# Performance work log

Measured on AMD Instinct MI355X. Metric: run time of the kernel, lower is better.

Reference implementation:

```python
import jax, jax.numpy as jnp
import numpy as np

N_NODES = 100000
N_EDGES = 1600000
IN_DIM = 128
HIDDEN = 128


def setup_inputs() -> dict:
    key = jax.random.key(0)
    k1, k2, k3 = jax.random.split(key, 3)
    x = jax.random.normal(k1, (N_NODES, IN_DIM), dtype=jnp.float32)
    edge_index = jax.random.randint(k2, (2, N_EDGES), 0, N_NODES, dtype=jnp.int64)
    # Glorot-ish init for the GCN weight
    W = jax.random.normal(k3, (IN_DIM, HIDDEN), dtype=jnp.float32) * (1.0 / np.sqrt(IN_DIM))
    b = jnp.zeros((HIDDEN,), dtype=jnp.float32)
    return {"x": x, "edge_index": edge_index, "W": W, "b": b}


def reference(x, edge_index, W, b):
    N = x.shape[0]
    # PyG GCNConv: add self-loops, symmetric deg^{-1/2} normalization,
    # linear transform, scatter-add aggregation at destination, + bias.
    loop = jnp.arange(N, dtype=edge_index.dtype)
    src = jnp.concatenate([edge_index[0], loop])
    dst = jnp.concatenate([edge_index[1], loop])

    ones = jnp.ones(src.shape[0], dtype=x.dtype)
    deg = jax.ops.segment_sum(ones, dst, num_segments=N)  # in-degree incl. self-loop
    dinv = jnp.where(deg > 0, jax.lax.rsqrt(deg), 0.0)
    norm = dinv[src] * dinv[dst]  # [E+N]

    xw = x @ W  # [N, H] dense transform first (GCNConv default)
    msgs = xw[src] * norm[:, None]  # gather + scale, [E+N, H]
    out = jax.ops.segment_sum(msgs, dst, num_segments=N) + b  # scatter-add
    return jax.nn.relu(out)
```

## Files before the change

### kernel.cpp

```cpp
#include <hip/hip_runtime.h>
#include <hip/hip_bf16.h>


#define SCAN_BLK 256
#define NP1 128
#define MAXB 1024

typedef short  short8 __attribute__((ext_vector_type(8)));
typedef float  f32x4  __attribute__((ext_vector_type(4)));

__device__ inline unsigned short f2b(float f) {
    unsigned u = __float_as_uint(f);
    return (unsigned short)((u + 0x7fffu + ((u >> 16) & 1u)) >> 16);
}

__device__ inline void acc4(float4& a, unsigned lo, unsigned hi) {
    a.x += __uint_as_float(lo << 16);
    a.y += __uint_as_float(lo & 0xffff0000u);
    a.z += __uint_as_float(hi << 16);
    a.w += __uint_as_float(hi & 0xffff0000u);
}

__global__ __launch_bounds__(256) void k_hist(const int* __restrict__ dst,
                                              int* __restrict__ hist,
                                              const float* __restrict__ W,
                                              unsigned short* __restrict__ Wt,
                                              int E, int B, int chunk) {
    __shared__ int h[MAXB];
    for (int i = threadIdx.x; i < B; i += 256) h[i] = 0;
    __syncthreads();
    int e0 = blockIdx.x * chunk;
    int e1 = min(E, e0 + chunk);
    for (int e = e0 + threadIdx.x; e < e1; e += 256)
        atomicAdd(&h[dst[e] >> 7], 1);
    __syncthreads();
    for (int i = threadIdx.x; i < B; i += 256)
        hist[i * NP1 + blockIdx.x] = h[i];
    if (blockIdx.x < 64) {
        int i = blockIdx.x * 256 + threadIdx.x;
        int k = i >> 7, n = i & 127;
        Wt[n * 128 + k] = f2b(W[k * 128 + n]);
    }
}

__global__ __launch_bounds__(SCAN_BLK) void k_scanA(const int* __restrict__ in,
                                                    int* __restrict__ bsum, int M) {
    __shared__ int s[SCAN_BLK];
    int t = threadIdx.x;
    int i = blockIdx.x * SCAN_BLK + t;
    s[t] = (i < M) ? in[i] : 0;
    __syncthreads();
    for (int off = SCAN_BLK / 2; off > 0; off >>= 1) {
        if (t < off) s[t] += s[t + off];
        __syncthreads();
    }
    if (t == 0) bsum[blockIdx.x] = s[0];
}

__global__ __launch_bounds__(512) void k_scanB(int* __restrict__ bsum, int nb) {
    __shared__ int s[512];
    int t = threadIdx.x;
    int v = (t < nb) ? bsum[t] : 0;
    s[t] = v;
    __syncthreads();
    for (int off = 1; off < 512; off <<= 1) {
        int add = (t >= off) ? s[t - off] : 0;
        __syncthreads();
        s[t] += add;
        __syncthreads();
    }
    if (t < nb) bsum[t] = s[t] - v;
}

__global__ __launch_bounds__(SCAN_BLK) void k_scanC2(int* __restrict__ data,
                                                     const int* __restrict__ bsum,
                                                     int M) {
    __shared__ int s[SCAN_BLK];
    int t = threadIdx.x;
    int i = blockIdx.x * SCAN_BLK + t;
    int v = (i < M) ? data[i] : 0;
    s[t] = v;
    __syncthreads();
    for (int off = 1; off < SCAN_BLK; off <<= 1) {
        int add = (t >= off) ? s[t - off] : 0;
        __syncthreads();
        s[t] += add;
        __syncthreads();
    }
    if (i < M) data[i] = s[t] - v + bsum[blockIdx.x];
}

__global__ __launch_bounds__(256) void k_scatter(const int* __restrict__ src,
                                                 const int* __restrict__ dst,
                                                 const int* __restrict__ hist_s,
                                                 unsigned* __restrict__ bucketed,
                                                 int E, int B, int chunk) {
    __shared__ int cur[MAXB];
    for (int i = threadIdx.x; i < B; i += 256)
        cur[i] = hist_s[i * NP1 + blockIdx.x];
    __syncthreads();
    int e0 = blockIdx.x * chunk;
    int e1 = min(E, e0 + chunk);
    for (int e = e0 + threadIdx.x; e < e1; e += 256) {
        int d = dst[e];
        int p = atomicAdd(&cur[d >> 7], 1);
        bucketed[p] = (unsigned)src[e] | ((unsigned)(d & 127) << 17);
    }
}

__global__ __launch_bounds__(256) void k_csr(const unsigned* __restrict__ bucketed,
                                             const int* __restrict__ hist_s,
                                             int* __restrict__ csr_src,
                                             int* __restrict__ rowptr,
                                             float* __restrict__ dinv_g,
                                             int E, int B, int N) {
    const int b = blockIdx.x;
    const int t = threadIdx.x;
    const int base = hist_s[b * NP1];
    const int endv = (b + 1 < B) ? hist_s[(b + 1) * NP1] : E;
    const int cnt = endv - base;
    const int node0 = b << 7;

    __shared__ int sdeg[128], sscan[128], cur[128];
    if (t < 128) sdeg[t] = 0;
    __syncthreads();
    for (int i = t; i < cnt; i += 256)
        atomicAdd(&sdeg[bucketed[base + i] >> 17], 1);
    __syncthreads();
    if (t < 128) sscan[t] = sdeg[t];
    __syncthreads();
    for (int off = 1; off < 128; off <<= 1) {
        int add = 0;
        if (t < 128 && t >= off) add = sscan[t - off];
        __syncthreads();
        if (t < 128) sscan[t] += add;
        __syncthreads();
    }
    if (t < 128) {
        int rs = sscan[t] - sdeg[t];
        cur[t] = rs;
        int node = node0 + t;
        if (node < N) {
            rowptr[node] = base + rs;
            dinv_g[node] = rsqrtf((float)(sdeg[t] + 1));
        }
    }
    if (b == B - 1 && t == 0) rowptr[N] = E;
    __syncthreads();
    for (int i = t; i < cnt; i += 256) {
        unsigned w = bucketed[base + i];
        int p = atomicAdd(&cur[w >> 17], 1);
        csr_src[base + p] = (int)(w & 0x1FFFFu);
    }
}

__global__ __launch_bounds__(256) void k_gemm(const float* __restrict__ x,
                                              const unsigned short* __restrict__ Wt,
                                              const float* __restrict__ dinv,
                                              unsigned* __restrict__ xs_out, int N) {
    __shared__ short out_lds[4][16][136];
    const int t = threadIdx.x;
    const int wv = t >> 6;
    const int lane = t & 63;
    const int quad = lane >> 4;
    const int lid = lane & 15;
    const int row0 = blockIdx.x * 64;

    int grow = row0 + wv * 16 + lid;
    int growc = grow < N ? grow : N - 1;
    short8 af[4];
#pragma unroll
    for (int q = 0; q < 4; ++q) {
        const float4* xr = (const float4*)(x + (size_t)growc * 128 + q * 32 + quad * 8);
        float4 f0 = xr[0], f1 = xr[1];
        af[q][0] = (short)f2b(f0.x); af[q][1] = (short)f2b(f0.y);
        af[q][2] = (short)f2b(f0.z); af[q][3] = (short)f2b(f0.w);
        af[q][4] = (short)f2b(f1.x); af[q][5] = (short)f2b(f1.y);
        af[q][6] = (short)f2b(f1.z); af[q][7] = (short)f2b(f1.w);
    }

    int drow = row0 + wv * 16 + quad * 4;
    float4 dv4;
    if (drow + 3 < N)      dv4 = *(const float4*)(dinv + drow);
    else {
        dv4.x = dinv[min(drow + 0, N - 1)];
        dv4.y = dinv[min(drow + 1, N - 1)];
        dv4.z = dinv[min(drow + 2, N - 1)];
        dv4.w = dinv[min(drow + 3, N - 1)];
    }

#pragma unroll
    for (int c = 0; c < 8; ++c) {
        f32x4 acc = {0.f, 0.f, 0.f, 0.f};
#pragma unroll
        for (int q = 0; q < 4; ++q) {
            const short8* bp = (const short8*)(Wt + (size_t)(c * 16 + lid) * 128 +
                                               q * 32 + quad * 8);
            acc = __builtin_amdgcn_mfma_f32_16x16x32_bf16(af[q], *bp, acc, 0, 0, 0);
        }
        out_lds[wv][quad * 4 + 0][c * 16 + lid] = (short)f2b(acc[0] * dv4.x);
        out_lds[wv][quad * 4 + 1][c * 16 + lid] = (short)f2b(acc[1] * dv4.y);
        out_lds[wv][quad * 4 + 2][c * 16 + lid] = (short)f2b(acc[2] * dv4.z);
        out_lds[wv][quad * 4 + 3][c * 16 + lid] = (short)f2b(acc[3] * dv4.w);
    }
    __syncthreads();

    int rl = lane >> 2;
    int cseg = lane & 3;
    int grow2 = row0 + wv * 16 + rl;
    if (grow2 < N) {
        uint4* dstp = (uint4*)(xs_out + (size_t)grow2 * 64);
        const uint4* srcp = (const uint4*)((const char*)&out_lds[wv][rl][0] + cseg * 64);
#pragma unroll
        for (int tt = 0; tt < 4; ++tt) dstp[cseg * 4 + tt] = srcp[tt];
    }
}

__global__ __launch_bounds__(256) void k_aggregate(const uint4* __restrict__ xs4,
                                                   const int* __restrict__ csr_src,
                                                   const int* __restrict__ rowptr,
                                                   const float* __restrict__ dinv,
                                                   const float* __restrict__ bias,
                                                   float* __restrict__ out, int N) {
    const int wave = threadIdx.x >> 6;
    const int lane = threadIdx.x & 63;
    const int g0 = (blockIdx.x * 4 + wave) * 4;
    if (g0 >= N) return;
    const int grp = lane >> 4;
    const int sub = lane & 15;

    int   rp  = rowptr[min(g0 + min(lane, 4), N)];
    float dvl = dinv[min(g0 + min(lane, 3), N - 1)];

    int rs[4], c[4], idx[4];
#pragma unroll
    for (int k = 0; k < 4; ++k) {
        rs[k] = __shfl(rp, k);
        c[k]  = __shfl(rp, k + 1) - rs[k];
    }
#pragma unroll
    for (int k = 0; k < 4; ++k)
        idx[k] = (lane < c[k]) ? csr_src[rs[k] + lane] : 0;

    const uint2* xs2 = (const uint2*)xs4;

#pragma unroll
    for (int k = 0; k < 4; ++k) {
        int n = g0 + k;
        if (n < N) {
            const int cc = c[k];
            float4 a0 = make_float4(0.f, 0.f, 0.f, 0.f);
            float4 a1 = make_float4(0.f, 0.f, 0.f, 0.f);
            int cmain = cc < 64 ? cc : 64;
            int jmax = (cmain + 3) >> 2;
            for (int j = 0; j < jmax; ++j) {
                int e = j * 4 + grp;
                int row = __shfl(idx[k], e & 63);
                uint4 u = xs4[(size_t)row * 16 + sub];
                if (e >= cc) { u.x = 0u; u.y = 0u; u.z = 0u; u.w = 0u; }
                acc4(a0, u.x, u.y);
                acc4(a1, u.z, u.w);
            }
            for (int e0 = 64; e0 < cc; e0 += 4) {
                int e = e0 + grp;
                uint4 u = make_uint4(0u, 0u, 0u, 0u);
                if (e < cc) {
                    int row = csr_src[rs[k] + e];
                    u = xs4[(size_t)row * 16 + sub];
                }
                acc4(a0, u.x, u.y);
                acc4(a1, u.z, u.w);
            }
            a0.x += __shfl_xor(a0.x, 16); a0.x += __shfl_xor(a0.x, 32);
            a0.y += __shfl_xor(a0.y, 16); a0.y += __shfl_xor(a0.y, 32);
            a0.z += __shfl_xor(a0.z, 16); a0.z += __shfl_xor(a0.z, 32);
            a0.w += __shfl_xor(a0.w, 16); a0.w += __shfl_xor(a0.w, 32);
            a1.x += __shfl_xor(a1.x, 16); a1.x += __shfl_xor(a1.x, 32);
            a1.y += __shfl_xor(a1.y, 16); a1.y += __shfl_xor(a1.y, 32);
            a1.z += __shfl_xor(a1.z, 16); a1.z += __shfl_xor(a1.z, 32);
            a1.w += __shfl_xor(a1.w, 16); a1.w += __shfl_xor(a1.w, 32);

            if (lane < 32) {
                int p = lane >> 4;
                int f4 = (lane & 15) * 2 + p;
                float4 av = p ? a1 : a0;
                uint2 su = xs2[(size_t)n * 32 + f4];
                acc4(av, su.x, su.y);
                float dv = __shfl(dvl, k);
                float4 bb = ((const float4*)bias)[f4];
                float4 o;
                o.x = fmaxf(dv * av.x + bb.x, 0.f);
                o.y = fmaxf(dv * av.y + bb.y, 0.f);
                o.z = fmaxf(dv * av.z + bb.z, 0.f);
                o.w = fmaxf(dv * av.w + bb.w, 0.f);
                ((float4*)(out + (size_t)n * 128))[f4] = o;
            }
        }
    }
}

extern "C" void kernel_launch(void* const* d_in, const int* in_sizes, int n_in,
                              void* d_out, int out_size, void* d_ws, size_t ws_size,
                              hipStream_t stream) {
    const float* x   = (const float*)d_in[0];
    const int*   ei  = (const int*)d_in[1];
    const float* W   = (const float*)d_in[2];
    const float* b   = (const float*)d_in[3];
    float*       out = (float*)d_out;

    const int N = in_sizes[0] / 128;
    const int E = in_sizes[1] / 2;
    const int* src = ei;
    const int* dst = ei + E;

    const int B = (N + 127) >> 7;
    const int M = B * NP1;
    const int chunk = (E + NP1 - 1) / NP1;

    auto align = [](size_t v) { return (v + 255) & ~(size_t)255; };
    char* p = (char*)d_ws;
    int*            hist     = (int*)p;            p += align((size_t)M * 4);
    int*            bsum     = (int*)p;            p += align(512 * 4);
    int*            rowptr   = (int*)p;            p += align(((size_t)N + 1) * 4);
    float*          dinv     = (float*)p;          p += align((size_t)N * 4);
    unsigned*       bucketed = (unsigned*)p;       p += align((size_t)E * 4);
    int*            csr_src  = (int*)p;            p += align((size_t)E * 4);
    unsigned*       xs       = (unsigned*)p;       p += align((size_t)N * 64 * 4);
    unsigned short* Wt       = (unsigned short*)p; p += align(128 * 128 * 2);
    (void)ws_size;

    const int nbM = (M + SCAN_BLK - 1) / SCAN_BLK;

    k_hist   <<<NP1, 256, 0, stream>>>(dst, hist, W, Wt, E, B, chunk);
    k_scanA  <<<nbM, 256, 0, stream>>>(hist, bsum, M);
    k_scanB  <<<1, 512, 0, stream>>>(bsum, nbM);
    k_scanC2 <<<nbM, 256, 0, stream>>>(hist, bsum, M);
    k_scatter<<<NP1, 256, 0, stream>>>(src, dst, hist, bucketed, E, B, chunk);
    k_csr    <<<B, 256, 0, stream>>>(bucketed, hist, csr_src, rowptr, dinv, E, B, N);
    k_gemm   <<<(N + 63) / 64, 256, 0, stream>>>(x, Wt, dinv, xs, N);
    k_aggregate<<<(N + 15) / 16, 256, 0, stream>>>((const uint4*)xs, csr_src, rowptr,
                                                   dinv, b, out, N);
}
```

Measured before the change: 261.7 us.

## Assign one node per wave in aggregate and unroll gathers by sixteen edges

The aggregation kernel now gives each wave a single destination node instead of four in sequence, so the grid is four times larger. The main gather loop is unrolled to issue four independent row loads per iteration, with a masked tail step for leftover edges. The goal is more memory-level parallelism and less serial latency per wave on the random gathers. In exchange, rowptr and dinv are read with per-wave scalar loads, more waves are launched, and nodes with very few edges still pay a full masked tail block.

```diff
diff --git a/kernel.cpp b/kernel.cpp
--- a/kernel.cpp
+++ b/kernel.cpp
@@ -224,78 +224,76 @@
                                                    float* __restrict__ out, int N) {
     const int wave = threadIdx.x >> 6;
     const int lane = threadIdx.x & 63;
-    const int g0 = (blockIdx.x * 4 + wave) * 4;
-    if (g0 >= N) return;
+    const int n = blockIdx.x * 4 + wave;
+    if (n >= N) return;
     const int grp = lane >> 4;
     const int sub = lane & 15;
 
-    int   rp  = rowptr[min(g0 + min(lane, 4), N)];
-    float dvl = dinv[min(g0 + min(lane, 3), N - 1)];
-
-    int rs[4], c[4], idx[4];
-#pragma unroll
-    for (int k = 0; k < 4; ++k) {
-        rs[k] = __shfl(rp, k);
-        c[k]  = __shfl(rp, k + 1) - rs[k];
-    }
-#pragma unroll
-    for (int k = 0; k < 4; ++k)
-        idx[k] = (lane < c[k]) ? csr_src[rs[k] + lane] : 0;
-
-    const uint2* xs2 = (const uint2*)xs4;
-
-#pragma unroll
-    for (int k = 0; k < 4; ++k) {
-        int n = g0 + k;
-        if (n < N) {
-            const int cc = c[k];
-            float4 a0 = make_float4(0.f, 0.f, 0.f, 0.f);
-            float4 a1 = make_float4(0.f, 0.f, 0.f, 0.f);
-            int cmain = cc < 64 ? cc : 64;
-            int jmax = (cmain + 3) >> 2;
-            for (int j = 0; j < jmax; ++j) {
-                int e = j * 4 + grp;
-                int row = __shfl(idx[k], e & 63);
-                uint4 u = xs4[(size_t)row * 16 + sub];
-                if (e >= cc) { u.x = 0u; u.y = 0u; u.z = 0u; u.w = 0u; }
-                acc4(a0, u.x, u.y);
-                acc4(a1, u.z, u.w);
-            }
-            for (int e0 = 64; e0 < cc; e0 += 4) {
-                int e = e0 + grp;
-                uint4 u = make_uint4(0u, 0u, 0u, 0u);
-                if (e < cc) {
-                    int row = csr_src[rs[k] + e];
-                    u = xs4[(size_t)row * 16 + sub];
-                }
-                acc4(a0, u.x, u.y);
-                acc4(a1, u.z, u.w);
-            }
-            a0.x += __shfl_xor(a0.x, 16); a0.x += __shfl_xor(a0.x, 32);
-            a0.y += __shfl_xor(a0.y, 16); a0.y += __shfl_xor(a0.y, 32);
-            a0.z += __shfl_xor(a0.z, 16); a0.z += __shfl_xor(a0.z, 32);
-            a0.w += __shfl_xor(a0.w, 16); a0.w += __shfl_xor(a0.w, 32);
-            a1.x += __shfl_xor(a1.x, 16); a1.x += __shfl_xor(a1.x, 32);
-            a1.y += __shfl_xor(a1.y, 16); a1.y += __shfl_xor(a1.y, 32);
-            a1.z += __shfl_xor(a1.z, 16); a1.z += __shfl_xor(a1.z, 32);
-            a1.w += __shfl_xor(a1.w, 16); a1.w += __shfl_xor(a1.w, 32);
-
-            if (lane < 32) {
-                int p = lane >> 4;
-                int f4 = (lane & 15) * 2 + p;
-                float4 av = p ? a1 : a0;
-                uint2 su = xs2[(size_t)n * 32 + f4];
-                acc4(av, su.x, su.y);
-                float dv = __shfl(dvl, k);
-                float4 bb = ((const float4*)bias)[f4];
-                float4 o;
-                o.x = fmaxf(dv * av.x + bb.x, 0.f);
-                o.y = fmaxf(dv * av.y + bb.y, 0.f);
-                o.z = fmaxf(dv * av.z + bb.z, 0.f);
-                o.w = fmaxf(dv * av.w + bb.w, 0.f);
-                ((float4*)(out + (size_t)n * 128))[f4] = o;
-            }
-        }
+    const int rs = rowptr[n];
+    const int c  = rowptr[n + 1] - rs;
+    const float dv = dinv[n];
+
+    int idxreg = (lane < c) ? csr_src[rs + lane] : 0;
+
+    float4 a0 = make_float4(0.f, 0.f, 0.f, 0.f);
+    float4 a1 = make_float4(0.f, 0.f, 0.f, 0.f);
+    const int cmain = c < 64 ? c : 64;
+
+    int i = 0;
+    for (; i + 16 <= cmain; i += 16) {
+#pragma unroll
+        for (int j = 0; j < 4; ++j) {
+            int row = __shfl(idxreg, i + 4 * j + grp);
+            uint4 u = xs4[(size_t)row * 16 + sub];
+            acc4(a0, u.x, u.y);
+            acc4(a1, u.z, u.w);
+        }
+    }
+    if (i < cmain) {
+#pragma unroll
+        for (int j = 0; j < 4; ++j) {
+            int e = i + 4 * j + grp;
+            int row = __shfl(idxreg, e);
+            uint4 u = xs4[(size_t)row * 16 + sub];
+            if (e >= cmain) { u.x = 0u; u.y = 0u; u.z = 0u; u.w = 0u; }
+            acc4(a0, u.x, u.y);
+            acc4(a1, u.z, u.w);
+        }
+    }
+    for (int e0 = 64; e0 < c; e0 += 4) {
+        int e = e0 + grp;
+        uint4 u = make_uint4(0u, 0u, 0u, 0u);
+        if (e < c) {
+            int row = csr_src[rs + e];
+            u = xs4[(size_t)row * 16 + sub];
+        }
+        acc4(a0, u.x, u.y);
+        acc4(a1, u.z, u.w);
+    }
+
+    a0.x += __shfl_xor(a0.x, 16); a0.x += __shfl_xor(a0.x, 32);
+    a0.y += __shfl_xor(a0.y, 16); a0.y += __shfl_xor(a0.y, 32);
+    a0.z += __shfl_xor(a0.z, 16); a0.z += __shfl_xor(a0.z, 32);
+    a0.w += __shfl_xor(a0.w, 16); a0.w += __shfl_xor(a0.w, 32);
+    a1.x += __shfl_xor(a1.x, 16); a1.x += __shfl_xor(a1.x, 32);
+    a1.y += __shfl_xor(a1.y, 16); a1.y += __shfl_xor(a1.y, 32);
+    a1.z += __shfl_xor(a1.z, 16); a1.z += __shfl_xor(a1.z, 32);
+    a1.w += __shfl_xor(a1.w, 16); a1.w += __shfl_xor(a1.w, 32);
+
+    if (lane < 32) {
+        const uint2* xs2 = (const uint2*)xs4;
+        int p = lane >> 4;
+        int f4 = (lane & 15) * 2 + p;
+        float4 av = p ? a1 : a0;
+        uint2 su = xs2[(size_t)n * 32 + f4];
+        acc4(av, su.x, su.y);
+        float4 bb = ((const float4*)bias)[f4];
+        float4 o;
+        o.x = fmaxf(dv * av.x + bb.x, 0.f);
+        o.y = fmaxf(dv * av.y + bb.y, 0.f);
+        o.z = fmaxf(dv * av.z + bb.z, 0.f);
+        o.w = fmaxf(dv * av.w + bb.w, 0.f);
+        ((float4*)(out + (size_t)n * 128))[f4] = o;
     }
 }
 
@@ -338,6 +336,6 @@
     k_scatter<<<NP1, 256, 0, stream>>>(src, dst, hist, bucketed, E, B, chunk);
     k_csr    <<<B, 256, 0, stream>>>(bucketed, hist, csr_src, rowptr, dinv, E, B, N);
     k_gemm   <<<(N + 63) / 64, 256, 0, stream>>>(x, Wt, dinv, xs, N);
-    k_aggregate<<<(N + 15) / 16, 256, 0, stream>>>((const uint4*)xs, csr_src, rowptr,
-                                                   dinv, b, out, N);
-}
+    k_aggregate<<<(N + 3) / 4, 256, 0, stream>>>((const uint4*)xs, csr_src, rowptr,
+                                                 dinv, b, out, N);
+}
```

Result: faster. 255.8 us (-2.2%).
